# Performance work log

Measured on AMD Instinct MI355X. Metric: run time of the kernel, lower is better.

## Reference

```python
import jax, jax.numpy as jnp
import numpy as np

D_MODEL = 1024
INNER = 2048      # expand=2
D_STATE = 16
D_CONV = 4
DT_RANK = 64      # ceil(1024/16)
DT_MIN, DT_MAX = 0.001, 0.1
RMS_EPS = 1e-6


def _causal_depthwise_conv1d(x, kernel, bias):
    # x: (B, L, C), kernel: (K, C)
    channels = x.shape[-1]
    rhs = kernel[:, None, :]  # (K, 1, C)
    out = jax.lax.conv_general_dilated(
        lhs=x, rhs=rhs, window_strides=(1,),
        padding=[(kernel.shape[0] - 1, 0)],
        dimension_numbers=("NWC", "WIO", "NWC"),
        feature_group_count=channels)
    return out + bias[None, None, :]


def _selective_scan(u, dt, b, c, a, d):
    # u, dt: (B, L, Di); b, c: (B, L, S); a: (Di, S); d: (Di,)
    da = jnp.exp(dt[..., None] * a)                  # (B, L, Di, S)
    db = (dt * u)[..., None] * b[:, :, None, :]      # (B, L, Di, S)

    def step(h, inp):
        da_t, db_t, c_t = inp
        h = da_t * h + db_t                          # (B, Di, S)
        y = jnp.einsum("bds,bs->bd", h, c_t)
        return h, y

    h0 = jnp.zeros((u.shape[0], u.shape[2], a.shape[1]), u.dtype)
    _, ys = jax.lax.scan(
        step, h0,
        (da.transpose(1, 0, 2, 3), db.transpose(1, 0, 2, 3), c.transpose(1, 0, 2)))
    return ys.transpose(1, 0, 2) + u * d             # (B, L, Di)


def setup_inputs() -> dict:
    key = jax.random.key(0)
    ks = jax.random.split(key, 16)

    def lin(k, fan_in, shape):
        return jax.random.normal(k, shape, jnp.float32) / np.sqrt(fan_in)

    a_init = jnp.log(jnp.arange(1, D_STATE + 1, dtype=jnp.float32))
    return {
        "x": jax.random.normal(ks[0], (2, 2048, D_MODEL), jnp.float32),
        "norm_scale": jnp.ones((D_MODEL,), jnp.float32),
        "in_proj_w": lin(ks[1], D_MODEL, (D_MODEL, 2 * INNER)),
        "in_proj_b": jnp.zeros((2 * INNER,), jnp.float32),
        "out_proj_w": lin(ks[2], INNER, (INNER, D_MODEL)),
        "out_proj_b": jnp.zeros((D_MODEL,), jnp.float32),
        "dt_in_w": lin(ks[3], INNER, (INNER, DT_RANK)),
        "dt_in_b": jnp.zeros((DT_RANK,), jnp.float32),
        "dt_out_w": lin(ks[4], DT_RANK, (DT_RANK, INNER)),
        "dt_out_b": jnp.zeros((INNER,), jnp.float32),
        "b_proj_w": lin(ks[5], INNER, (INNER, D_STATE)),
        "b_proj_b": jnp.zeros((D_STATE,), jnp.float32),
        "c_proj_w": lin(ks[6], INNER, (INNER, D_STATE)),
        "c_proj_b": jnp.zeros((D_STATE,), jnp.float32),
        "conv_kernel": jax.random.normal(ks[7], (D_CONV, INNER), jnp.float32) / np.sqrt(D_CONV),
        "conv_bias": jnp.zeros((INNER,), jnp.float32),
        "a_log": jnp.tile(a_init[None, :], (INNER, 1)),
        "d": jnp.ones((INNER,), jnp.float32),
        "dt_bias": jnp.zeros((INNER,), jnp.float32),
    }


def reference(x, norm_scale, in_proj_w, in_proj_b, out_proj_w, out_proj_b,
              dt_in_w, dt_in_b, dt_out_w, dt_out_b, b_proj_w, b_proj_b,
              c_proj_w, c_proj_b, conv_kernel, conv_bias, a_log, d, dt_bias):
    residual = x
    # RMSNorm
    var = jnp.mean(jnp.square(x), axis=-1, keepdims=True)
    xn = x * jax.lax.rsqrt(var + RMS_EPS) * norm_scale
    # in projection -> u, z
    uz = xn @ in_proj_w + in_proj_b
    u, z = jnp.split(uz, 2, axis=-1)
    # causal depthwise conv + silu
    u = _causal_depthwise_conv1d(u, conv_kernel, conv_bias)
    u = jax.nn.silu(u)
    # dt path (low-rank) -> softplus -> clip
    dt = (u @ dt_in_w + dt_in_b) @ dt_out_w + dt_out_b + dt_bias
    dt = jnp.clip(jax.nn.softplus(dt), DT_MIN, DT_MAX)
    # B, C projections with tanh
    b = jnp.tanh(u @ b_proj_w + b_proj_b)
    c = jnp.tanh(u @ c_proj_w + c_proj_b)
    # selective scan
    a = -jnp.exp(a_log)
    y = _selective_scan(u, dt, b, c, a, d)
    # gate, out projection, residual
    y = y * jax.nn.silu(z)
    y = y @ out_proj_w + out_proj_b
    return residual + y
```

## Files before the change

kernel.cpp:

```cpp
#include <hip/hip_runtime.h>
#include <cstdint>
#include <cstddef>

typedef unsigned short u16;
typedef __bf16 bf16x8 __attribute__((ext_vector_type(8)));
typedef float f32x4 __attribute__((ext_vector_type(4)));
typedef u16 u16x4 __attribute__((ext_vector_type(4)));

#define DMODEL 1024
#define DINNER 2048
#define NBATCH 2
#define LSEQ   2048
#define NTOK   4096
#define NSTATE 16
#define NCH    64
#define TCH    32

__device__ __forceinline__ u16 f2b(float f) {
  union { float f; unsigned u; } a; a.f = f;
  unsigned r = a.u + 0x7fffu + ((a.u >> 16) & 1u);
  return (u16)(r >> 16);
}
__device__ __forceinline__ float b2f(u16 h) {
  union { unsigned u; float f; } a; a.u = ((unsigned)h) << 16;
  return a.f;
}

__device__ __forceinline__ void gload_lds16(const u16* g, __bf16* l) {
  __builtin_amdgcn_global_load_lds(
      (const __attribute__((address_space(1))) unsigned int*)g,
      (__attribute__((address_space(3))) unsigned int*)l, 16, 0, 0);
}

__device__ __forceinline__ void pow16(float w, float* p) {
  p[0] = w;
  p[1] = p[0] * p[0];
  p[2] = p[1] * p[0];
  p[3] = p[1] * p[1];
  p[4] = p[3] * p[0];
  p[5] = p[3] * p[1];
  p[6] = p[3] * p[2];
  p[7] = p[3] * p[3];
  p[8]  = p[7] * p[0];
  p[9]  = p[7] * p[1];
  p[10] = p[7] * p[2];
  p[11] = p[7] * p[3];
  p[12] = p[7] * p[4];
  p[13] = p[7] * p[5];
  p[14] = p[7] * p[6];
  p[15] = p[7] * p[7];
}

__global__ __launch_bounds__(256)
void prep_all(const float* __restrict__ w_in, const float* __restrict__ w_out,
              const float* __restrict__ w_dti, const float* __restrict__ w_b,
              const float* __restrict__ w_c, const float* __restrict__ w_dto,
              const float* __restrict__ b_dto, const float* __restrict__ dtbias,
              const float* __restrict__ x, const float* __restrict__ nscale,
              u16* __restrict__ WINT, u16* __restrict__ WOUTT, u16* __restrict__ WBC,
              u16* __restrict__ WDT2T, float* __restrict__ DTB2, u16* __restrict__ XN) {
  __shared__ float sh[32 * 33];
  const int tid = threadIdx.x;
  const int xx = tid & 31, y0 = tid >> 5;
  int blk = blockIdx.x;
  if (blk < 4096) {
    int c0 = (blk & 127) * 32, r0 = (blk >> 7) * 32;
    #pragma unroll
    for (int yy = y0; yy < 32; yy += 8) sh[yy * 33 + xx] = w_in[(size_t)(r0 + yy) * 4096 + c0 + xx];
    __syncthreads();
    #pragma unroll
    for (int yy = y0; yy < 32; yy += 8) WINT[(size_t)(c0 + yy) * 1024 + r0 + xx] = f2b(sh[xx * 33 + yy]);
    return;
  }
  blk -= 4096;
  if (blk < 2048) {
    int c0 = (blk & 31) * 32, r0 = (blk >> 5) * 32;
    #pragma unroll
    for (int yy = y0; yy < 32; yy += 8) sh[yy * 33 + xx] = w_out[(size_t)(r0 + yy) * 1024 + c0 + xx];
    __syncthreads();
    #pragma unroll
    for (int yy = y0; yy < 32; yy += 8) WOUTT[(size_t)(c0 + yy) * 2048 + r0 + xx] = f2b(sh[xx * 33 + yy]);
    return;
  }
  blk -= 2048;
  if (blk < 192) {
    int c0 = (blk % 3) * 32, r0 = (blk / 3) * 32;
    #pragma unroll
    for (int yy = y0; yy < 32; yy += 8) {
      int r = r0 + yy, c = c0 + xx;
      float v = (c < 64) ? w_dti[(size_t)r * 64 + c]
                         : (c < 80 ? w_b[(size_t)r * 16 + (c - 64)] : w_c[(size_t)r * 16 + (c - 80)]);
      sh[yy * 33 + xx] = v;
    }
    __syncthreads();
    #pragma unroll
    for (int yy = y0; yy < 32; yy += 8) WBC[(size_t)(c0 + yy) * 2048 + r0 + xx] = f2b(sh[xx * 33 + yy]);
    return;
  }
  blk -= 192;
  if (blk < 128) {
    int c0 = (blk & 63) * 32, r0 = (blk >> 6) * 32;
    #pragma unroll
    for (int yy = y0; yy < 32; yy += 8) sh[yy * 33 + xx] = w_dto[(size_t)(r0 + yy) * 2048 + c0 + xx];
    __syncthreads();
    #pragma unroll
    for (int yy = y0; yy < 32; yy += 8) WDT2T[(size_t)(c0 + yy) * 64 + r0 + xx] = f2b(sh[xx * 33 + yy]);
    return;
  }
  blk -= 128;
  if (blk < 8) {
    int i = blk * 256 + tid;
    DTB2[i] = b_dto[i] + dtbias[i];
    return;
  }
  blk -= 8;
  {
    const float4* xp = (const float4*)(x + (size_t)blk * DMODEL);
    float4 v = xp[tid];
    float ss = v.x * v.x + v.y * v.y + v.z * v.z + v.w * v.w;
    #pragma unroll
    for (int o = 32; o; o >>= 1) ss += __shfl_down(ss, o);
    if ((tid & 63) == 0) sh[tid >> 6] = ss;
    __syncthreads();
    float tot = sh[0] + sh[1] + sh[2] + sh[3];
    float r = rsqrtf(tot * (1.0f / DMODEL) + 1e-6f);
    float4 sc = ((const float4*)nscale)[tid];
    u16x4 o4;
    o4[0] = f2b(v.x * r * sc.x); o4[1] = f2b(v.y * r * sc.y);
    o4[2] = f2b(v.z * r * sc.z); o4[3] = f2b(v.w * r * sc.w);
    *(u16x4*)(XN + (size_t)blk * DMODEL + tid * 4) = o4;
  }
}

__global__ __launch_bounds__(512, 1)
void gemm8p(const u16* __restrict__ A, const u16* __restrict__ Bt,
            const float* __restrict__ bias, u16* __restrict__ out,
            int M, int N, int K, int RM, int RN) {
  __shared__ __bf16 lds[65536];
  const int tid = threadIdx.x;
  const int lane = tid & 63;
  const int wave = tid >> 6;
  const int wr = wave >> 2, wc = wave & 3;

  const int GM = M >> 8;
  const int bid = blockIdx.x;
  const int xcd = bid & 7;
  const int l = bid >> 3;
  const int rgm = GM / RM;
  const int rr = xcd % rgm, rc = xcd / rgm;
  const size_t m0 = (size_t)(rr * RM + (l % RM)) * 256;
  const size_t n0 = (size_t)(rc * RN + (l / RM)) * 256;
  const int NT = K >> 6;

  const int st_kk = ((tid & 7) * 8) ^ (((tid >> 3) & 7) << 3);

#define SHALF(bufi, mat, half, kt, SRC, BASE)                                  \
  { _Pragma("unroll") for (int ss = 0; ss < 2; ss++) {                         \
      const int row_ = (tid >> 3) + ss * 64;                                   \
      gload_lds16(SRC + ((BASE) + (half) * 128 + row_) * K + (size_t)(kt) * 64 + st_kk, \
                  &lds[((bufi) * 2 + (mat)) * 16384 + (half) * 8192 + tid * 8 + ss * 4096]); } }

  f32x4 acc[8][4] = {};
  SHALF(0, 0, 0, 0, A,  m0)  SHALF(0, 1, 0, 0, Bt, n0)
  SHALF(0, 0, 1, 0, A,  m0)  SHALF(0, 1, 1, 0, Bt, n0)
  if (NT > 1) { SHALF(1, 0, 0, 1, A, m0)  SHALF(1, 1, 0, 1, Bt, n0) }

  const int rsw = (lane & 7) << 3;
  const int kgrp = (lane >> 4) * 8;
  const int arl = wr * 64 + (lane & 15);
  const int brl = wc * 32 + (lane & 15);

  bf16x8 af[2][4], bv[2][2];

#define DSA(QR)                                                                \
  { _Pragma("unroll") for (int ks = 0; ks < 2; ks++)                           \
      _Pragma("unroll") for (int i = 0; i < 4; i++)                            \
        af[ks][i] = *(const bf16x8*)(&lds[cur * 32768 + (QR) * 8192 +          \
                      (arl + i * 16) * 64 + ((ks * 32 + kgrp) ^ rsw)]); }
#define DSB(QC)                                                                \
  { _Pragma("unroll") for (int ks = 0; ks < 2; ks++)                           \
      _Pragma("unroll") for (int j = 0; j < 2; j++)                            \
        bv[ks][j] = *(const bf16x8*)(&lds[cur * 32768 + 16384 + (QC) * 8192 +  \
                      (brl + j * 16) * 64 + ((ks * 32 + kgrp) ^ rsw)]); }
#define MMA(QR, QC)                                                            \
  __builtin_amdgcn_s_barrier();                                                \
  asm volatile("s_waitcnt lgkmcnt(0)" ::: "memory");                           \
  __builtin_amdgcn_sched_barrier(0);                                           \
  __builtin_amdgcn_s_setprio(1);                                               \
  { _Pragma("unroll") for (int ks = 0; ks < 2; ks++)                           \
      _Pragma("unroll") for (int i = 0; i < 4; i++)                            \
        _Pragma("unroll") for (int j = 0; j < 2; j++)                          \
          acc[(QR) * 4 + i][(QC) * 2 + j] = __builtin_amdgcn_mfma_f32_16x16x32_bf16( \
              af[ks][i], bv[ks][j], acc[(QR) * 4 + i][(QC) * 2 + j], 0, 0, 0); } \
  __builtin_amdgcn_s_setprio(0);                                               \
  __builtin_amdgcn_sched_barrier(0);                                           \
  __builtin_amdgcn_s_barrier();                                                \
  asm volatile("" ::: "memory");

  for (int t = 0; t < NT; t++) {
    const int cur = t & 1;
    if (t == NT - 1) asm volatile("s_waitcnt vmcnt(0)" ::: "memory");
    else             asm volatile("s_waitcnt vmcnt(4)" ::: "memory");
    __builtin_amdgcn_s_barrier();
    asm volatile("" ::: "memory");
    DSA(0) DSB(0)
    if (t + 1 < NT) { SHALF(cur ^ 1, 0, 1, t + 1, A, m0) }
    MMA(0, 0)
    DSB(1)
    if (t + 1 < NT) { SHALF(cur ^ 1, 1, 1, t + 1, Bt, n0) }
    MMA(0, 1)
    DSA(1) DSB(0)
    if (t + 2 < NT) { SHALF(cur, 0, 0, t + 2, A, m0) }
    MMA(1, 0)
    DSB(1)
    if (t + 2 < NT) { SHALF(cur, 1, 0, t + 2, Bt, n0) }
    MMA(1, 1)
  }

  const int cr = (lane >> 4) << 2;
  const int cc = lane & 15;
  #pragma unroll
  for (int fr = 0; fr < 8; fr++) {
    #pragma unroll
    for (int fc = 0; fc < 4; fc++) {
      const size_t col = n0 + wc * 32 + (fc >> 1) * 128 + (fc & 1) * 16 + cc;
      const float bvs = bias[col];
      #pragma unroll
      for (int r = 0; r < 4; r++) {
        const size_t row = m0 + wr * 64 + (fr >> 2) * 128 + (fr & 3) * 16 + cr + r;
        out[row * N + col] = f2b(acc[fr][fc][r] + bvs);
      }
    }
  }
#undef SHALF
#undef DSA
#undef DSB
#undef MMA
}

template <int BM, int BN, int NWM, int NWN, int EPI>
__global__ __launch_bounds__(NWM * NWN * 64, 1)
void gemm_db(const u16* __restrict__ A, const u16* __restrict__ Bt,
             const float* __restrict__ bias, const float* __restrict__ res,
             void* __restrict__ outv, int M, int N, int K, int RM, int RN) {
  constexpr int NTHR = NWM * NWN * 64;
  constexpr int WMW = BM / NWM;
  constexpr int WNW = BN / NWN;
  constexpr int MF = WMW / 16;
  constexpr int NF = WNW / 16;
  constexpr int LPT = (BM + BN) * 8 / NTHR;
  __shared__ __bf16 lds[2][(BM + BN) * 64];
  const int tid = threadIdx.x;
  const int lane = tid & 63;
  const int wave = tid >> 6;
  const int wr = wave / NWN, wc = wave % NWN;

  const int GM = M / BM;
  const int bid = blockIdx.x;
  const int xcd = bid & 7;
  const int l = bid >> 3;
  const int rgm = GM / RM;
  const int rr = xcd % rgm, rc = xcd / rgm;
  const size_t m0 = (size_t)(rr * RM + (l % RM)) * BM;
  const size_t n0 = (size_t)(rc * RN + (l / RM)) * BN;
  const int NT = K >> 6;

#define STAGE_DB(bufi, k0)                                                     \
  { _Pragma("unroll")                                                          \
    for (int ss = 0; ss < BM * 8 / NTHR; ss++) {                               \
      int g = tid + ss * NTHR;                                                 \
      int row = g >> 3;                                                        \
      int kk = ((g & 7) * 8) ^ ((row & 7) << 3);                               \
      gload_lds16(A + (m0 + row) * K + (k0) + kk, &lds[bufi][g * 8]);          \
    }                                                                          \
    _Pragma("unroll")                                                          \
    for (int ss = 0; ss < BN * 8 / NTHR; ss++) {                               \
      int g = tid + ss * NTHR;                                                 \
      int row = g >> 3;                                                        \
      int kk = ((g & 7) * 8) ^ ((row & 7) << 3);                               \
      gload_lds16(Bt + (n0 + row) * K + (k0) + kk,                             \
                  &lds[bufi][BM * 64 + g * 8]);                                \
    } }

  f32x4 acc[MF][NF] = {};
  STAGE_DB(0, 0)
  STAGE_DB(1, 64)

  const int rsw = (lane & 7) << 3;
  const int arow0 = wr * WMW + (lane & 15);
  const int brow0 = wc * WNW + (lane & 15);
  const int kgrp = (lane >> 4) * 8;

  for (int t = 0; t < NT; t++) {
    const int cur = t & 1;
    if (t == NT - 1) asm volatile("s_waitcnt vmcnt(0)" ::: "memory");
    else             asm volatile("s_waitcnt vmcnt(%0)" :: "n"(LPT) : "memory");
    __builtin_amdgcn_s_barrier();
    asm volatile("" ::: "memory");
    const __bf16* As_ = &lds[cur][0];
    const __bf16* Bs_ = &lds[cur][BM * 64];
    #pragma unroll
    for (int qr = 0; qr < MF / 4; qr++) {
      #pragma unroll
      for (int qc = 0; qc < NF / 2; qc++) {
        bf16x8 af[2][4], bfv[2][2];
        #pragma unroll
        for (int ks = 0; ks < 2; ks++) {
          const int kk = (ks * 32 + kgrp) ^ rsw;
          #pragma unroll
          for (int i = 0; i < 4; i++)
            af[ks][i] = *(const bf16x8*)(As_ + (size_t)(arow0 + (qr * 4 + i) * 16) * 64 + kk);
          #pragma unroll
          for (int j = 0; j < 2; j++)
            bfv[ks][j] = *(const bf16x8*)(Bs_ + (size_t)(brow0 + (qc * 2 + j) * 16) * 64 + kk);
        }
        __builtin_amdgcn_s_setprio(1);
        #pragma unroll
        for (int ks = 0; ks < 2; ks++)
          #pragma unroll
          for (int i = 0; i < 4; i++)
            #pragma unroll
            for (int j = 0; j < 2; j++)
              acc[qr * 4 + i][qc * 2 + j] = __builtin_amdgcn_mfma_f32_16x16x32_bf16(
                  af[ks][i], bfv[ks][j], acc[qr * 4 + i][qc * 2 + j], 0, 0, 0);
        __builtin_amdgcn_s_setprio(0);
        __builtin_amdgcn_sched_barrier(0);
      }
    }
    __builtin_amdgcn_s_barrier();
    asm volatile("" ::: "memory");
    if (t + 2 < NT) { STAGE_DB(cur, (t + 2) * 64) }
  }

  const int cr = (lane >> 4) << 2;
  const int cc = lane & 15;
  #pragma unroll
  for (int fr = 0; fr < MF; fr++) {
    #pragma unroll
    for (int fc = 0; fc < NF; fc++) {
      const size_t col = n0 + wc * WNW + fc * 16 + cc;
      const float bv = bias[col];
      #pragma unroll
      for (int r = 0; r < 4; r++) {
        const size_t row = m0 + wr * WMW + fr * 16 + cr + r;
        if constexpr (EPI == 0) {
          ((u16*)outv)[row * N + col] = f2b(acc[fr][fc][r] + bv);
        } else {
          ((float*)outv)[row * N + col] = acc[fr][fc][r] + bv + res[row * N + col];
        }
      }
    }
  }
#undef STAGE_DB
}

template <int EPI, int BN>
__global__ __launch_bounds__(256)
void gemm_bt(const u16* __restrict__ A, const u16* __restrict__ Bt,
             const float* __restrict__ bias, const float* __restrict__ res,
             void* __restrict__ outv, int M, int N, int K, int ksplit) {
  constexpr int WN = BN / 2;
  constexpr int JN = WN / 16;
  __shared__ __bf16 As[128][72];
  __shared__ __bf16 Bs[BN][72];
  const int tid = threadIdx.x;
  const int m0 = blockIdx.y * 128;
  const int n0 = blockIdx.x * BN;
  const int wave = tid >> 6, lane = tid & 63;
  const int wm = (wave >> 1) * 64, wn = (wave & 1) * WN;
  const int sr = tid >> 3;
  const int sc = (tid & 7) * 8;
  const int kbeg = blockIdx.z * ksplit, kend = kbeg + ksplit;
  f32x4 acc[4][JN] = {};
  for (int k0 = kbeg; k0 < kend; k0 += 64) {
    __syncthreads();
    #pragma unroll
    for (int r = 0; r < 128; r += 32)
      *(bf16x8*)&As[sr + r][sc] = *(const bf16x8*)(A + (size_t)(m0 + sr + r) * K + k0 + sc);
    #pragma unroll
    for (int r = 0; r < BN; r += 32)
      *(bf16x8*)&Bs[sr + r][sc] = *(const bf16x8*)(Bt + (size_t)(n0 + sr + r) * K + k0 + sc);
    __syncthreads();
    #pragma unroll
    for (int ks = 0; ks < 64; ks += 32) {
      const int kr = ks + ((lane >> 4) << 3);
      bf16x8 af[4], bfr[JN];
      #pragma unroll
      for (int i = 0; i < 4; i++) af[i]  = *(const bf16x8*)&As[wm + (lane & 15) + i * 16][kr];
      #pragma unroll
      for (int j = 0; j < JN; j++) bfr[j] = *(const bf16x8*)&Bs[wn + (lane & 15) + j * 16][kr];
      #pragma unroll
      for (int i = 0; i < 4; i++)
        #pragma unroll
        for (int j = 0; j < JN; j++)
          acc[i][j] = __builtin_amdgcn_mfma_f32_16x16x32_bf16(af[i], bfr[j], acc[i][j], 0, 0, 0);
    }
  }
  const int cr = (lane >> 4) << 2;
  const int cc = lane & 15;
  #pragma unroll
  for (int i = 0; i < 4; i++) {
    #pragma unroll
    for (int j = 0; j < JN; j++) {
      const int col = n0 + wn + j * 16 + cc;
      #pragma unroll
      for (int r = 0; r < 4; r++) {
        const int row = m0 + wm + i * 16 + cr + r;
        float v = acc[i][j][r];
        if constexpr (EPI == 1) {
          ((float*)outv)[(size_t)blockIdx.z * M * N + (size_t)row * N + col] = v;
        } else {
          v += bias[col];
          v = (v > 20.0f) ? v : log1pf(__expf(v));
          v = fminf(fmaxf(v, 0.001f), 0.1f);
          ((u16*)outv)[(size_t)row * N + col] = f2b(v);
        }
      }
    }
  }
}

__global__ __launch_bounds__(256)
void conv_silu_seq(const u16* __restrict__ uz, const float* __restrict__ ck,
                   const float* __restrict__ cb, u16* __restrict__ u) {
  int d  = (blockIdx.x & 7) * 256 + threadIdx.x;
  int lc = (blockIdx.x >> 3) & 127;
  int b  = blockIdx.x >> 10;
  const float w0 = ck[d], w1 = ck[DINNER + d], w2 = ck[2 * DINNER + d], w3 = ck[3 * DINNER + d];
  const float bias = cb[d];
  const int t0 = lc * 16;
  float x0 = 0.f, x1 = 0.f, x2 = 0.f;
  #pragma unroll
  for (int j = -3; j < 0; j++) {
    int t = t0 + j;
    float v = (t >= 0) ? b2f(uz[((size_t)(b * LSEQ + t)) * (2 * DINNER) + d]) : 0.f;
    x0 = x1; x1 = x2; x2 = v;
  }
  #pragma unroll
  for (int i = 0; i < 16; i++) {
    int t = t0 + i;
    float x3 = b2f(uz[((size_t)(b * LSEQ + t)) * (2 * DINNER) + d]);
    float acc = bias + w0 * x0 + w1 * x1 + w2 * x2 + w3 * x3;
    float sv = acc / (1.0f + __expf(-acc));
    u[((size_t)(b * LSEQ + t)) * DINNER + d] = f2b(sv);
    x0 = x1; x1 = x2; x2 = x3;
  }
}

__global__ __launch_bounds__(256)
void prep_dtbc(const float* __restrict__ dtbc, const float* __restrict__ dtin_b,
               const float* __restrict__ bb, const float* __restrict__ cbias,
               u16* __restrict__ dt1, float* __restrict__ Bm, float* __restrict__ Cm) {
  int idx = blockIdx.x * 256 + threadIdx.x;
  if (idx >= NTOK * 96) return;
  int row = idx / 96, col = idx - row * 96;
  float v = 0.f;
  #pragma unroll
  for (int z = 0; z < 8; z++)
    v += dtbc[(size_t)z * NTOK * 96 + (size_t)row * 96 + col];
  if (col < 64)       dt1[(size_t)row * 64 + col] = f2b(v + dtin_b[col]);
  else if (col < 80)  Bm[(size_t)row * NSTATE + col - 64] = tanhf(v + bb[col - 64]);
  else                Cm[(size_t)row * NSTATE + col - 80] = tanhf(v + cbias[col - 80]);
}

__global__ __launch_bounds__(256)
void scan_pass1(const u16* __restrict__ dt, const u16* __restrict__ u,
                const float* __restrict__ Bm, const float* __restrict__ alog,
                float* __restrict__ chP, float* __restrict__ chS) {
  const int d  = (blockIdx.x & 7) * 256 + threadIdx.x;
  const int ch = (blockIdx.x >> 3) & (NCH - 1);
  const int b  = blockIdx.x >> 9;
  float A[NSTATE];
  #pragma unroll
  for (int s = 0; s < NSTATE; s++) A[s] = -__expf(alog[(size_t)d * NSTATE + s]);
  const float A0 = A[0];
  bool structured = true;
  #pragma unroll
  for (int s = 1; s < NSTATE; s++)
    structured = structured && (fabsf(A[s] - (s + 1) * A0) <= 1e-4f * fabsf((s + 1) * A0));
  float h[NSTATE];
  #pragma unroll
  for (int s = 0; s < NSTATE; s++) h[s] = 0.0f;
  const int t0 = ch * TCH;
  size_t base = (((size_t)b * NCH + ch) * DINNER + d) * NSTATE;
  if (structured) {
    float sdt = 0.f;
    for (int i = 0; i < TCH; i++) {
      const size_t tok = (size_t)b * LSEQ + t0 + i;
      float dtv = b2f(dt[tok * DINNER + d]);
      float uv  = b2f(u[tok * DINNER + d]);
      float dtu = dtv * uv;
      const float* bp = Bm + tok * NSTATE;
      sdt += dtv;
      float p[NSTATE];
      pow16(__expf(dtv * A0), p);
      #pragma unroll
      for (int s = 0; s < NSTATE; s++) h[s] = p[s] * h[s] + dtu * bp[s];
    }
    float P[NSTATE];
    pow16(__expf(sdt * A0), P);
    #pragma unroll
    for (int s = 0; s < NSTATE; s++) { chP[base + s] = P[s]; chS[base + s] = h[s]; }
  } else {
    float P[NSTATE];
    #pragma unroll
    for (int s = 0; s < NSTATE; s++) P[s] = 1.0f;
    for (int i = 0; i < TCH; i++) {
      const size_t tok = (size_t)b * LSEQ + t0 + i;
      float dtv = b2f(dt[tok * DINNER + d]);
      float uv  = b2f(u[tok * DINNER + d]);
      float dtu = dtv * uv;
      const float* bp = Bm + tok * NSTATE;
      #pragma unroll
      for (int s = 0; s < NSTATE; s++) {
        float da = __expf(dtv * A[s]);
        P[s] *= da;
        h[s] = da * h[s] + dtu * bp[s];
      }
    }
    #pragma unroll
    for (int s = 0; s < NSTATE; s++) { chP[base + s] = P[s]; chS[base + s] = h[s]; }
  }
}

__global__ __launch_bounds__(256)
void scan_pass2(const float* __restrict__ chP, const float* __restrict__ chS,
                float* __restrict__ hst) {
  const int b   = blockIdx.x >> 7;
  const int off = (blockIdx.x & 127) * 256 + threadIdx.x;
  float h = 0.f;
  const size_t stride = (size_t)DINNER * NSTATE;
  size_t base = (size_t)b * NCH * stride + off;
  for (int c = 0; c < NCH; c++) {
    size_t a = base + (size_t)c * stride;
    float P = chP[a], S = chS[a];
    hst[a] = h;
    h = P * h + S;
  }
}

__global__ __launch_bounds__(256)
void scan_pass3(const u16* __restrict__ dt, const u16* __restrict__ u,
                const float* __restrict__ Bm, const float* __restrict__ Cm,
                const float* __restrict__ alog, const float* __restrict__ dvec,
                const u16* __restrict__ uz, const float* __restrict__ hst,
                u16* __restrict__ y) {
  const int d  = (blockIdx.x & 7) * 256 + threadIdx.x;
  const int ch = (blockIdx.x >> 3) & (NCH - 1);
  const int b  = blockIdx.x >> 9;
  float A[NSTATE];
  #pragma unroll
  for (int s = 0; s < NSTATE; s++) A[s] = -__expf(alog[(size_t)d * NSTATE + s]);
  const float A0 = A[0];
  bool structured = true;
  #pragma unroll
  for (int s = 1; s < NSTATE; s++)
    structured = structured && (fabsf(A[s] - (s + 1) * A0) <= 1e-4f * fabsf((s + 1) * A0));
  float h[NSTATE];
  const size_t hbase = (((size_t)b * NCH + ch) * DINNER + d) * NSTATE;
  #pragma unroll
  for (int s = 0; s < NSTATE; s++) h[s] = hst[hbase + s];
  const float dval = dvec[d];
  const int t0 = ch * TCH;
  if (structured) {
    for (int i = 0; i < TCH; i++) {
      const size_t tok = (size_t)b * LSEQ + t0 + i;
      float dtv = b2f(dt[tok * DINNER + d]);
      float uv  = b2f(u[tok * DINNER + d]);
      float dtu = dtv * uv;
      const float* bp = Bm + tok * NSTATE;
      const float* cp = Cm + tok * NSTATE;
      float p[NSTATE];
      pow16(__expf(dtv * A0), p);
      float yv = 0.0f;
      #pragma unroll
      for (int s = 0; s < NSTATE; s++) {
        h[s] = p[s] * h[s] + dtu * bp[s];
        yv += h[s] * cp[s];
      }
      yv += uv * dval;
      float z = b2f(uz[tok * (2 * DINNER) + DINNER + d]);
      float g = z / (1.0f + __expf(-z));
      y[tok * DINNER + d] = f2b(yv * g);
    }
  } else {
    for (int i = 0; i < TCH; i++) {
      const size_t tok = (size_t)b * LSEQ + t0 + i;
      float dtv = b2f(dt[tok * DINNER + d]);
      float uv  = b2f(u[tok * DINNER + d]);
      float dtu = dtv * uv;
      const float* bp = Bm + tok * NSTATE;
      const float* cp = Cm + tok * NSTATE;
      float yv = 0.0f;
      #pragma unroll
      for (int s = 0; s < NSTATE; s++) {
        float da = __expf(dtv * A[s]);
        h[s] = da * h[s] + dtu * bp[s];
        yv += h[s] * cp[s];
      }
      yv += uv * dval;
      float z = b2f(uz[tok * (2 * DINNER) + DINNER + d]);
      float g = z / (1.0f + __expf(-z));
      y[tok * DINNER + d] = f2b(yv * g);
    }
  }
}

#define WS_XN     ((size_t)0)
#define WS_WINT   (WS_XN     + 8388608)
#define WS_CHP    ((size_t)0)
#define WS_WOUTT  (WS_WINT   + 8388608)
#define WS_WBC    (WS_WOUTT  + 4194304)
#define WS_WDT2T  (WS_WBC    + 524288)
#define WS_DT1    (WS_WDT2T  + 262144)
#define WS_DTB2   (WS_DT1    + 524288)
#define WS_BMAT   (WS_DTB2   + 8192)
#define WS_CMAT   (WS_BMAT   + 262144)
#define WS_UZ     (WS_CMAT   + 262144)
#define WS_U      (WS_UZ     + 33554432)
#define WS_DTBC   (WS_U      + 16777216)
#define WS_DT     (WS_DTBC   + 16777216)
#define WS_CHS    (WS_DT     + 16777216)
#define WS_YBF    (WS_CHS    + 16777216)

extern "C" void kernel_launch(void* const* d_in, const int* in_sizes, int n_in,
                              void* d_out, int out_size, void* d_ws, size_t ws_size,
                              hipStream_t stream) {
  const float* x      = (const float*)d_in[0];
  const float* nscale = (const float*)d_in[1];
  const float* w_in   = (const float*)d_in[2];
  const float* b_in   = (const float*)d_in[3];
  const float* w_out  = (const float*)d_in[4];
  const float* b_out  = (const float*)d_in[5];
  const float* w_dti  = (const float*)d_in[6];
  const float* b_dti  = (const float*)d_in[7];
  const float* w_dto  = (const float*)d_in[8];
  const float* b_dto  = (const float*)d_in[9];
  const float* w_b    = (const float*)d_in[10];
  const float* b_b    = (const float*)d_in[11];
  const float* w_c    = (const float*)d_in[12];
  const float* b_c    = (const float*)d_in[13];
  const float* convk  = (const float*)d_in[14];
  const float* convb  = (const float*)d_in[15];
  const float* alog   = (const float*)d_in[16];
  const float* dvec   = (const float*)d_in[17];
  const float* dtbias = (const float*)d_in[18];
  float* out = (float*)d_out;
  char* ws = (char*)d_ws;

  u16*  XN    = (u16*)(ws + WS_XN);
  u16*  WINT  = (u16*)(ws + WS_WINT);
  u16*  WOUTT = (u16*)(ws + WS_WOUTT);
  u16*  WBC   = (u16*)(ws + WS_WBC);
  u16*  WDT2T = (u16*)(ws + WS_WDT2T);
  u16*  DT1   = (u16*)(ws + WS_DT1);
  float* DTB2 = (float*)(ws + WS_DTB2);
  float* BMAT = (float*)(ws + WS_BMAT);
  float* CMAT = (float*)(ws + WS_CMAT);
  u16*  UZ    = (u16*)(ws + WS_UZ);
  u16*  U     = (u16*)(ws + WS_U);
  float* DTBC = (float*)(ws + WS_DTBC);
  u16*  DT    = (u16*)(ws + WS_DT);
  float* CHP  = (float*)(ws + WS_CHP);
  float* CHS  = (float*)(ws + WS_CHS);
  float* HST  = (float*)(ws + WS_CHS);
  u16*  YBF   = (u16*)(ws + WS_YBF);

  prep_all<<<10568, 256, 0, stream>>>(w_in, w_out, w_dti, w_b, w_c, w_dto,
                                      b_dto, dtbias, x, nscale,
                                      WINT, WOUTT, WBC, WDT2T, DTB2, XN);

  gemm8p<<<256, 512, 0, stream>>>(XN, WINT, b_in, UZ, NTOK, 4096, 1024, 4, 8);

  conv_silu_seq<<<NBATCH * 128 * 8, 256, 0, stream>>>(UZ, convk, convb, U);

  gemm_bt<1, 96><<<dim3(1, NTOK / 128, 8), 256, 0, stream>>>(
      U, WBC, nullptr, nullptr, DTBC, NTOK, 96, 2048, 256);
  prep_dtbc<<<(NTOK * 96 + 255) / 256, 256, 0, stream>>>(DTBC, b_dti, b_b, b_c, DT1, BMAT, CMAT);

  gemm_bt<2, 128><<<dim3(2048 / 128, NTOK / 128, 1), 256, 0, stream>>>(
      DT1, WDT2T, DTB2, nullptr, DT, NTOK, 2048, 64, 64);

  scan_pass1<<<NBATCH * NCH * 8, 256, 0, stream>>>(DT, U, BMAT, alog, CHP, CHS);
  scan_pass2<<<NBATCH * 128, 256, 0, stream>>>(CHP, CHS, HST);
  scan_pass3<<<NBATCH * NCH * 8, 256, 0, stream>>>(DT, U, BMAT, CMAT, alog, dvec, UZ, HST, YBF);

  gemm_db<128, 128, 2, 2, 3><<<256, 256, 0, stream>>>(
      YBF, WOUTT, b_out, x, out, NTOK, 1024, 2048, 4, 8);
}
```

Baseline: 206.6 us.

## Stage GEMM epilogue through LDS, relax vmcnt waits, compress scan chunk decay

The first GEMM's epilogue now writes bf16 results into LDS and then stores them with coalesced 16-byte row writes, replacing scattered 2-byte global stores. The load pipeline waits are split into vmcnt(8) and vmcnt(6) so more prefetches stay in flight. scan_pass1 stores a single per-channel decay scalar instead of 16 chunk products, and scan_pass2 rebuilds the powers from it. A NaN sentinel selects the fallback path when A is not structured. This cuts scan traffic in exchange for extra LDS barriers and a new workspace buffer.

```diff
diff --git a/kernel.cpp b/kernel.cpp
--- a/kernel.cpp
+++ b/kernel.cpp
@@ -200,12 +200,13 @@
   for (int t = 0; t < NT; t++) {
     const int cur = t & 1;
     if (t == NT - 1) asm volatile("s_waitcnt vmcnt(0)" ::: "memory");
-    else             asm volatile("s_waitcnt vmcnt(4)" ::: "memory");
+    else             asm volatile("s_waitcnt vmcnt(8)" ::: "memory");
     __builtin_amdgcn_s_barrier();
     asm volatile("" ::: "memory");
     DSA(0) DSB(0)
     if (t + 1 < NT) { SHALF(cur ^ 1, 0, 1, t + 1, A, m0) }
     MMA(0, 0)
+    if (t < NT - 1) asm volatile("s_waitcnt vmcnt(6)" ::: "memory");
     DSB(1)
     if (t + 1 < NT) { SHALF(cur ^ 1, 1, 1, t + 1, Bt, n0) }
     MMA(0, 1)
@@ -217,19 +218,31 @@
     MMA(1, 1)
   }
 
+  u16* eps = (u16*)lds;
   const int cr = (lane >> 4) << 2;
   const int cc = lane & 15;
   #pragma unroll
-  for (int fr = 0; fr < 8; fr++) {
-    #pragma unroll
-    for (int fc = 0; fc < 4; fc++) {
-      const size_t col = n0 + wc * 32 + (fc >> 1) * 128 + (fc & 1) * 16 + cc;
-      const float bvs = bias[col];
-      #pragma unroll
-      for (int r = 0; r < 4; r++) {
-        const size_t row = m0 + wr * 64 + (fr >> 2) * 128 + (fr & 3) * 16 + cr + r;
-        out[row * N + col] = f2b(acc[fr][fc][r] + bvs);
+  for (int g = 0; g < 2; g++) {
+    __syncthreads();
+    #pragma unroll
+    for (int fr4 = 0; fr4 < 4; fr4++) {
+      const int lrow = wr * 64 + fr4 * 16 + cr;
+      #pragma unroll
+      for (int fc = 0; fc < 4; fc++) {
+        const int lcol = wc * 32 + (fc >> 1) * 128 + (fc & 1) * 16 + cc;
+        const float bvs = bias[n0 + lcol];
+        #pragma unroll
+        for (int r = 0; r < 4; r++)
+          eps[(lrow + r) * 264 + lcol] = f2b(acc[g * 4 + fr4][fc][r] + bvs);
       }
+    }
+    __syncthreads();
+    #pragma unroll
+    for (int p = 0; p < 8; p++) {
+      const int row = (tid >> 5) + p * 16;
+      const int col = (tid & 31) * 8;
+      bf16x8 v = *(const bf16x8*)&eps[row * 264 + col];
+      *(bf16x8*)&out[(m0 + g * 128 + row) * N + n0 + col] = v;
     }
   }
 #undef SHALF
@@ -466,7 +479,8 @@
 __global__ __launch_bounds__(256)
 void scan_pass1(const u16* __restrict__ dt, const u16* __restrict__ u,
                 const float* __restrict__ Bm, const float* __restrict__ alog,
-                float* __restrict__ chP, float* __restrict__ chS) {
+                float* __restrict__ chP, float* __restrict__ chS,
+                float* __restrict__ chW) {
   const int d  = (blockIdx.x & 7) * 256 + threadIdx.x;
   const int ch = (blockIdx.x >> 3) & (NCH - 1);
   const int b  = blockIdx.x >> 9;
@@ -483,6 +497,7 @@
   for (int s = 0; s < NSTATE; s++) h[s] = 0.0f;
   const int t0 = ch * TCH;
   size_t base = (((size_t)b * NCH + ch) * DINNER + d) * NSTATE;
+  size_t wbase = ((size_t)b * NCH + ch) * DINNER + d;
   if (structured) {
     float sdt = 0.f;
     for (int i = 0; i < TCH; i++) {
@@ -497,10 +512,9 @@
       #pragma unroll
       for (int s = 0; s < NSTATE; s++) h[s] = p[s] * h[s] + dtu * bp[s];
     }
-    float P[NSTATE];
-    pow16(__expf(sdt * A0), P);
-    #pragma unroll
-    for (int s = 0; s < NSTATE; s++) { chP[base + s] = P[s]; chS[base + s] = h[s]; }
+    chW[wbase] = __expf(sdt * A0);
+    #pragma unroll
+    for (int s = 0; s < NSTATE; s++) chS[base + s] = h[s];
   } else {
     float P[NSTATE];
     #pragma unroll
@@ -518,6 +532,7 @@
         h[s] = da * h[s] + dtu * bp[s];
       }
     }
+    chW[wbase] = __int_as_float(0x7fc00000);
     #pragma unroll
     for (int s = 0; s < NSTATE; s++) { chP[base + s] = P[s]; chS[base + s] = h[s]; }
   }
@@ -525,15 +540,28 @@
 
 __global__ __launch_bounds__(256)
 void scan_pass2(const float* __restrict__ chP, const float* __restrict__ chS,
-                float* __restrict__ hst) {
+                const float* __restrict__ chW, float* __restrict__ hst) {
   const int b   = blockIdx.x >> 7;
   const int off = (blockIdx.x & 127) * 256 + threadIdx.x;
+  const int s   = off & 15;
+  const int d   = off >> 4;
+  const int e   = s + 1;
   float h = 0.f;
   const size_t stride = (size_t)DINNER * NSTATE;
   size_t base = (size_t)b * NCH * stride + off;
+  size_t wb   = (size_t)b * NCH * DINNER + d;
   for (int c = 0; c < NCH; c++) {
     size_t a = base + (size_t)c * stride;
-    float P = chP[a], S = chS[a];
+    float w = chW[wb + (size_t)c * DINNER];
+    float P;
+    if (__builtin_isnan(w)) {
+      P = chP[a];
+    } else {
+      float W2 = w * w, W4 = W2 * W2, W8 = W4 * W4;
+      P = ((e & 1) ? w : 1.f) * ((e & 2) ? W2 : 1.f) * ((e & 4) ? W4 : 1.f)
+        * ((e & 8) ? W8 : 1.f) * ((e & 16) ? W8 * W8 : 1.f);
+    }
+    float S = chS[a];
     hst[a] = h;
     h = P * h + S;
   }
@@ -622,6 +650,7 @@
 #define WS_DT     (WS_DTBC   + 16777216)
 #define WS_CHS    (WS_DT     + 16777216)
 #define WS_YBF    (WS_CHS    + 16777216)
+#define WS_CHW    (WS_YBF    + 16777216)
 
 extern "C" void kernel_launch(void* const* d_in, const int* in_sizes, int n_in,
                               void* d_out, int out_size, void* d_ws, size_t ws_size,
@@ -665,6 +694,7 @@
   float* CHS  = (float*)(ws + WS_CHS);
   float* HST  = (float*)(ws + WS_CHS);
   u16*  YBF   = (u16*)(ws + WS_YBF);
+  float* CHW  = (float*)(ws + WS_CHW);
 
   prep_all<<<10568, 256, 0, stream>>>(w_in, w_out, w_dti, w_b, w_c, w_dto,
                                       b_dto, dtbias, x, nscale,
@@ -681,8 +711,8 @@
   gemm_bt<2, 128><<<dim3(2048 / 128, NTOK / 128, 1), 256, 0, stream>>>(
       DT1, WDT2T, DTB2, nullptr, DT, NTOK, 2048, 64, 64);
 
-  scan_pass1<<<NBATCH * NCH * 8, 256, 0, stream>>>(DT, U, BMAT, alog, CHP, CHS);
-  scan_pass2<<<NBATCH * 128, 256, 0, stream>>>(CHP, CHS, HST);
+  scan_pass1<<<NBATCH * NCH * 8, 256, 0, stream>>>(DT, U, BMAT, alog, CHP, CHS, CHW);
+  scan_pass2<<<NBATCH * 128, 256, 0, stream>>>(CHP, CHS, CHW, HST);
   scan_pass3<<<NBATCH * NCH * 8, 256, 0, stream>>>(DT, U, BMAT, CMAT, alog, dvec, UZ, HST, YBF);
 
   gemm_db<128, 128, 2, 2, 3><<<256, 256, 0, stream>>>(
```

Measured after the change: 219.3 us. 6.1% more time.
